# Optimization experiments

Measured on AMD Instinct MI355X. Metric: run time of the kernel, lower is better.

The kernel has to match this reference:

```python
import jax, jax.numpy as jnp
import numpy as np

# RCGANConfig constants
D_X, D_EPS = 64, 16
A_VOCAB, A_EMB = 100, 32
T_VOCAB, T_EMB = 4, 16
D_H = 128
D_IN = A_EMB + T_EMB + D_X + D_EPS + 1  # 129 (use_prev_y adds 1)


def setup_inputs() -> dict:
    key = jax.random.key(0)
    ks = jax.random.split(key, 20)
    B, T = 1024, 256
    s = 0.05
    x = jax.random.normal(ks[0], (B, D_X), jnp.float32)
    a = jax.random.randint(ks[1], (B, T), 0, A_VOCAB, jnp.int32)
    t = jax.random.randint(ks[2], (B, T), 0, T_VOCAB, jnp.int32)
    y = (jax.random.uniform(ks[3], (B, T)) < 0.5).astype(jnp.float32)
    mask = jnp.ones((B, T), jnp.float32)
    eps = jax.random.normal(ks[4], (B, T, D_EPS), jnp.float32)
    # parameters
    Wx = jax.random.normal(ks[5], (D_X, D_X), jnp.float32) * s
    bx = jnp.zeros((D_X,), jnp.float32)
    Ea = jax.random.normal(ks[6], (A_VOCAB, A_EMB), jnp.float32) * s
    Et = jax.random.normal(ks[7], (T_VOCAB, T_EMB), jnp.float32) * s
    Wih = jax.random.normal(ks[8], (3 * D_H, D_IN), jnp.float32) * s
    Whh = jax.random.normal(ks[9], (3 * D_H, D_H), jnp.float32) * s
    bih = jnp.zeros((3 * D_H,), jnp.float32)
    bhh = jnp.zeros((3 * D_H,), jnp.float32)
    W0 = jax.random.normal(ks[10], (D_H, D_X + D_EPS), jnp.float32) * s
    b0 = jnp.zeros((D_H,), jnp.float32)
    Wy = jax.random.normal(ks[11], (1, D_H), jnp.float32) * s
    by = jnp.zeros((1,), jnp.float32)
    return {"x": x, "a": a, "t": t, "y": y, "mask": mask, "eps": eps,
            "Wx": Wx, "bx": bx, "Ea": Ea, "Et": Et, "Wih": Wih, "Whh": Whh,
            "bih": bih, "bhh": bhh, "W0": W0, "b0": b0, "Wy": Wy, "by": by}


def reference(x, a, t, y, mask, eps, Wx, bx, Ea, Et, Wih, Whh, bih, bhh, W0, b0, Wy, by):
    # teacher_forcing path, rnn='gru', use_prev_y=True, y provided, stochastic_y=False
    B, T = a.shape
    x_enc = x @ Wx.T + bx                                        # [B, d_x] (constant per step)
    h0 = jnp.tanh(jnp.concatenate([x_enc, eps[:, 0, :]], -1) @ W0.T + b0)  # [B, d_h]
    # prev_y: zeros at t=0, then detached teacher signal y[:, t-1]
    prev_y = jnp.concatenate(
        [jnp.zeros((B, 1), y.dtype), jax.lax.stop_gradient(y[:, :-1])], axis=1)[..., None]  # [B,T,1]
    a_enc = Ea[a]                                                # [B,T,a_emb]
    t_enc = Et[t]                                                # [B,T,t_emb]
    inp = jnp.concatenate(
        [a_enc, t_enc, jnp.broadcast_to(x_enc[:, None, :], (B, T, x_enc.shape[-1])), eps, prev_y],
        axis=-1)                                                 # [B,T,d_in]
    gates_x = inp @ Wih.T + bih                                  # [B,T,3*d_h] precomputed input gates

    def step(h, gx):
        gh = h @ Whh.T + bhh
        gx_r, gx_z, gx_n = jnp.split(gx, 3, axis=-1)
        gh_r, gh_z, gh_n = jnp.split(gh, 3, axis=-1)
        r = jax.nn.sigmoid(gx_r + gh_r)
        z = jax.nn.sigmoid(gx_z + gh_z)
        n = jnp.tanh(gx_n + r * gh_n)
        h_new = (1.0 - z) * n + z * h
        return h_new, h_new

    _, hs = jax.lax.scan(step, h0, jnp.swapaxes(gates_x, 0, 1))  # hs: [T,B,d_h]
    hs = jnp.swapaxes(hs, 0, 1)                                  # [B,T,d_h]
    logits = hs @ Wy.T + by                                      # [B,T,1]
    prob = jax.nn.sigmoid(logits)
    m = mask[..., None]
    logits_o = m * logits + (1.0 - m) * jax.lax.stop_gradient(logits)
    y_o = m * prob + (1.0 - m) * jax.lax.stop_gradient(prob)
    # stacked: [..., 0] = y_logits, [..., 1] = y
    return jnp.concatenate([logits_o, y_o], axis=-1)             # [B,T,2]
```

## Files before the change

kernel.cpp:

```cpp
#include <hip/hip_runtime.h>
#include <hip/hip_bf16.h>

typedef __attribute__((ext_vector_type(8))) short bfrag;
typedef __attribute__((ext_vector_type(4))) float ffrag;

#define NB 1024
#define NT 256

#define KSIG -1.44269504f
#define KTAN -2.88539008f

static __device__ __forceinline__ float fast_rcp(float x) { return __builtin_amdgcn_rcpf(x); }
static __device__ __forceinline__ float sigm(float x) {
  return fast_rcp(1.f + __builtin_amdgcn_exp2f(-1.44269504f * x));
}
static __device__ __forceinline__ float sigm_pre(float s) {
  return fast_rcp(1.f + __builtin_amdgcn_exp2f(s));
}
static __device__ __forceinline__ float tanh_pre(float s) {
  return __builtin_fmaf(2.f, fast_rcp(1.f + __builtin_amdgcn_exp2f(s)), -1.f);
}
static __device__ __forceinline__ float tanh_f(float x) {
  return __builtin_fmaf(2.f, fast_rcp(1.f + __builtin_amdgcn_exp2f(-2.88539008f * x)), -1.f);
}
static __device__ __forceinline__ float bf2f(__hip_bfloat16 v) { return __bfloat162float(v); }
static __device__ __forceinline__ short f2bs(float f) {
  __hip_bfloat16 h = __float2bfloat16(f);
  return *reinterpret_cast<short*>(&h);
}
static __device__ __forceinline__ void barrier_lgkm() {
  asm volatile("s_waitcnt lgkmcnt(0)\n\ts_barrier" ::: "memory");
}

__global__ __launch_bounds__(512, 2) void gru_kernel(
    const float* __restrict__ x,
    const int* __restrict__ a_ids,
    const int* __restrict__ t_ids,
    const float* __restrict__ y,
    const float* __restrict__ eps,
    const float* __restrict__ Wx,
    const float* __restrict__ bx,
    const float* __restrict__ Ea,
    const float* __restrict__ Et,
    const float* __restrict__ Wih,
    const float* __restrict__ Whh,
    const float* __restrict__ bih,
    const float* __restrict__ bhh,
    const float* __restrict__ W0,
    const float* __restrict__ b0g,
    const float* __restrict__ Wy,
    const float* __restrict__ by,
    float* __restrict__ out)
{
  __shared__ __align__(16) __hip_bfloat16 h_bf[2][16][136];
  __shared__ __align__(16) __hip_bfloat16 Ea_s[100][40];
  __shared__ __align__(16) __hip_bfloat16 Et_s[4][16];
  __shared__ float prevy_s[2][16];
  __shared__ float bsum_r[128], bsum_z[128], bihn_s[128], bhhn_s[128];
  __shared__ float wprev_s[384];
  __shared__ __align__(16) char uni[38912];
  unsigned short* id_s    = (unsigned short*)(uni);
  __hip_bfloat16* eps_ch  = (__hip_bfloat16*)(uni + 8192);
  float*          y_ch    = (float*)(uni + 32768);
  __hip_bfloat16* Wxb     = (__hip_bfloat16*)(uni);
  __hip_bfloat16* W0b     = (__hip_bfloat16*)(uni + 8192);
  float*          x_s     = (float*)(uni + 28672);
  float*          eps0s   = (float*)(uni + 32832);
  float*          xe_s    = (float*)(uni + 33920);
  float*          h0f     = (float*)(uni);

  const int tid = threadIdx.x;
  const int w = tid >> 6, l = tid & 63;
  const int lmod = l & 15, ldiv = l >> 4;
  const int i_own = 16 * w + lmod;
  const int b0 = blockIdx.x * 16;

  if (tid < 128) {
    bsum_r[tid] = KSIG * (bih[tid] + bhh[tid]);
    bsum_z[tid] = KSIG * (bih[128 + tid] + bhh[128 + tid]);
    bihn_s[tid] = KTAN * bih[256 + tid];
    bhhn_s[tid] = KTAN * bhh[256 + tid];
  }
  if (tid < 384) wprev_s[tid] = ((tid < 256) ? KSIG : KTAN) * Wih[tid * 129 + 128];
  for (int j = tid; j < 3200; j += 512) {
    int r = j >> 5, c = j & 31;
    Ea_s[r][c] = __float2bfloat16(Ea[j]);
  }
  if (tid < 64) ((__hip_bfloat16*)Et_s)[tid] = __float2bfloat16(Et[tid]);
  for (int j = tid; j < 4096; j += 512)  Wxb[j] = __float2bfloat16(Wx[j]);
  for (int j = tid; j < 10240; j += 512) W0b[j] = __float2bfloat16(W0[j]);
  for (int j = tid; j < 1024; j += 512) {
    int r = j >> 6, c = j & 63;
    x_s[r * 65 + c] = x[(b0 + r) * 64 + c];
  }
  if (tid < 256) {
    int r = tid >> 4, c = tid & 15;
    eps0s[r * 17 + c] = eps[((b0 + r) * NT) * 16 + c];
  }
  const float by_f = by[0];

  bfrag Bh[3][4], Bi[3][2];
  #pragma unroll
  for (int g = 0; g < 3; g++) {
    const float sg = (g < 2) ? KSIG : KTAN;
    int n = (g * 8 + w) * 16 + lmod;
    #pragma unroll
    for (int kc = 0; kc < 4; kc++) {
      int k = kc * 32 + ldiv * 8;
      const float* wh = Whh + n * 128 + k;
      float4 h0v = *reinterpret_cast<const float4*>(wh);
      float4 h1v = *reinterpret_cast<const float4*>(wh + 4);
      bfrag th = {f2bs(sg * h0v.x), f2bs(sg * h0v.y), f2bs(sg * h0v.z), f2bs(sg * h0v.w),
                  f2bs(sg * h1v.x), f2bs(sg * h1v.y), f2bs(sg * h1v.z), f2bs(sg * h1v.w)};
      Bh[g][kc] = th;
    }
    #pragma unroll
    for (int kc = 0; kc < 2; kc++) {
      bfrag ti;
      #pragma unroll
      for (int j = 0; j < 8; j++) {
        int dk = kc * 32 + ldiv * 8 + j;
        int col = dk < 48 ? dk : dk + 64;
        ti[j] = f2bs(sg * Wih[n * 129 + col]);
      }
      Bi[g][kc] = ti;
    }
  }
  bfrag Bl[4];
  if (w == 7) {
    #pragma unroll
    for (int kc = 0; kc < 4; kc++) {
      bfrag bt;
      #pragma unroll
      for (int j = 0; j < 8; j++)
        bt[j] = (lmod == 0) ? f2bs(Wy[kc * 32 + ldiv * 8 + j]) : (short)0;
      Bl[kc] = bt;
    }
  }
  __syncthreads();

  for (int j = tid; j < 1024; j += 512) {
    int r = j & 15, i = j >> 4;
    float acc = bx[i];
    #pragma unroll 8
    for (int k = 0; k < 64; k++) acc += x_s[r * 65 + k] * bf2f(Wxb[i * 64 + k]);
    xe_s[r * 65 + i] = acc;
    h_bf[1][r][i] = __float2bfloat16(acc);
  }
  __syncthreads();

  for (int j = tid; j < 2048; j += 512) {
    int r = j & 15, o = j >> 4;
    float acc = b0g[o];
    #pragma unroll 8
    for (int k = 0; k < 64; k++) acc += xe_s[r * 65 + k] * bf2f(W0b[o * 80 + k]);
    #pragma unroll
    for (int k = 0; k < 16; k++) acc += eps0s[r * 17 + k] * bf2f(W0b[o * 80 + 64 + k]);
    h0f[r * 128 + o] = tanh_f(acc);
  }

  ffrag gxc[3];
  {
    ffrag z = {0.f, 0.f, 0.f, 0.f};
    gxc[0] = z; gxc[1] = z; gxc[2] = z;
    #pragma unroll
    for (int kc = 0; kc < 2; kc++) {
      bfrag axd = *reinterpret_cast<const bfrag*>(&h_bf[1][lmod][kc * 32 + ldiv * 8]);
      #pragma unroll
      for (int g = 0; g < 3; g++) {
        const float sg = (g < 2) ? KSIG : KTAN;
        int n = (g * 8 + w) * 16 + lmod;
        const float* wi = Wih + n * 129 + 48 + kc * 32 + ldiv * 8;
        bfrag bt;
        #pragma unroll
        for (int j = 0; j < 8; j++) bt[j] = f2bs(sg * wi[j]);
        gxc[g] = __builtin_amdgcn_mfma_f32_16x16x32_bf16(axd, bt, gxc[g], 0, 0, 0);
      }
    }
    float brf = bsum_r[i_own], bzf = bsum_z[i_own], bn1 = bihn_s[i_own];
    #pragma unroll
    for (int q = 0; q < 4; q++) {
      gxc[0][q] += brf;
      gxc[1][q] += bzf;
      gxc[2][q] += bn1;
    }
  }
  __syncthreads();

  float h_reg[4];
  #pragma unroll
  for (int q = 0; q < 4; q++) {
    int row = ldiv * 4 + q;
    float hv = h0f[row * 128 + i_own];
    h_reg[q] = hv;
    h_bf[0][row][i_own] = __float2bfloat16(hv);
  }
  __syncthreads();

  for (int j = tid; j < 4096; j += 512) {
    int r = j >> 8, t = j & 255;
    unsigned short v = (unsigned short)(a_ids[(b0 + r) * NT + t] |
                                        (t_ids[(b0 + r) * NT + t] << 8));
    id_s[t * 16 + r] = v;
  }
  {
    int r = tid >> 5, sub = tid & 31;
    const float* p = eps + ((b0 + r) * NT) * 16 + sub * 8;
    float4 eA = *reinterpret_cast<const float4*>(p);
    float4 eB = *reinterpret_cast<const float4*>(p + 4);
    int toff = sub >> 1, c8 = (sub & 1) * 8;
    bfrag e = {f2bs(eA.x), f2bs(eA.y), f2bs(eA.z), f2bs(eA.w),
               f2bs(eB.x), f2bs(eB.y), f2bs(eB.z), f2bs(eB.w)};
    *reinterpret_cast<bfrag*>(&eps_ch[(toff * 16 + r) * 24 + c8]) = e;
    if (tid < 64) {
      int r2 = tid >> 2, s2 = tid & 3;
      float4 yv = *reinterpret_cast<const float4*>(y + (b0 + r2) * NT + s2 * 4);
      *reinterpret_cast<float4*>(&y_ch[r2 * 16 + s2 * 4]) = yv;
    }
  }
  if (tid < 16) prevy_s[0][tid] = 0.f;
  const float wpr = wprev_s[i_own], wpz = wprev_s[128 + i_own], wpn = wprev_s[256 + i_own];
  const float bn2 = bhhn_s[i_own];
  const char* const ea_base  = (const char*)Ea_s + ldiv * 16;
  const char* const et_base  = (const char*)Et_s + ldiv * 16;
  const char* const eps_base = (const char*)eps_ch + lmod * 48 + (ldiv - 2) * 16;
  __syncthreads();

  ffrag pa0 = gxc[0], pa1 = gxc[1], pa2 = gxc[2];
  {
    int id = id_s[lmod];
    int aid = id & 127, tv = id >> 8;
    bfrag axA = *reinterpret_cast<const bfrag*>(ea_base + aid * 80);
    const char* etp = et_base + tv * 32;
    const char* epp = eps_base;
    bfrag axB = *reinterpret_cast<const bfrag*>(ldiv < 2 ? etp : epp);
    pa0 = __builtin_amdgcn_mfma_f32_16x16x32_bf16(axA, Bi[0][0], pa0, 0, 0, 0);
    pa1 = __builtin_amdgcn_mfma_f32_16x16x32_bf16(axA, Bi[1][0], pa1, 0, 0, 0);
    pa2 = __builtin_amdgcn_mfma_f32_16x16x32_bf16(axA, Bi[2][0], pa2, 0, 0, 0);
    pa0 = __builtin_amdgcn_mfma_f32_16x16x32_bf16(axB, Bi[0][1], pa0, 0, 0, 0);
    pa1 = __builtin_amdgcn_mfma_f32_16x16x32_bf16(axB, Bi[1][1], pa1, 0, 0, 0);
    pa2 = __builtin_amdgcn_mfma_f32_16x16x32_bf16(axB, Bi[2][1], pa2, 0, 0, 0);
  }

  for (int t = 0; t < NT; t++) {
    const int buf = t & 1, nbuf = buf ^ 1;

    const bool ck = ((t & 15) == 0) && (t + 16 < NT);
    float4 eA, eB, yv;
    const int cr = tid >> 5, csub = tid & 31;
    if (ck) {
      const float* p = eps + ((b0 + cr) * NT + t + 16) * 16 + csub * 8;
      eA = *reinterpret_cast<const float4*>(p);
      eB = *reinterpret_cast<const float4*>(p + 4);
      if (tid < 64) {
        int r2 = tid >> 2, s2 = tid & 3;
        yv = *reinterpret_cast<const float4*>(y + (b0 + r2) * NT + t + 16 + s2 * 4);
      }
    }

    ffrag anh, agl;
    #pragma unroll
    for (int q = 0; q < 4; q++) anh[q] = bn2;
    if (w == 7) {
      #pragma unroll
      for (int q = 0; q < 4; q++) agl[q] = by_f;
    }
    #pragma unroll
    for (int kc = 0; kc < 4; kc++) {
      bfrag ah = *reinterpret_cast<const bfrag*>(&h_bf[buf][lmod][kc * 32 + ldiv * 8]);
      pa0 = __builtin_amdgcn_mfma_f32_16x16x32_bf16(ah, Bh[0][kc], pa0, 0, 0, 0);
      pa1 = __builtin_amdgcn_mfma_f32_16x16x32_bf16(ah, Bh[1][kc], pa1, 0, 0, 0);
      anh = __builtin_amdgcn_mfma_f32_16x16x32_bf16(ah, Bh[2][kc], anh, 0, 0, 0);
      if (w == 7)
        agl = __builtin_amdgcn_mfma_f32_16x16x32_bf16(ah, Bl[kc], agl, 0, 0, 0);
    }

    if (tid >= 384 && tid < 400) {
      int r = tid - 384;
      prevy_s[nbuf][r] = y_ch[((t >> 4) & 1) * 256 + r * 16 + (t & 15)];
    }

    if (w == 7 && t > 0 && lmod == 0) {
      #pragma unroll
      for (int q = 0; q < 4; q++) {
        int row = ldiv * 4 + q;
        float lg = agl[q];
        float2 v;
        v.x = lg;
        v.y = sigm(lg);
        *reinterpret_cast<float2*>(out + ((b0 + row) * NT + (t - 1)) * 2) = v;
      }
    }

    #pragma unroll
    for (int q = 0; q < 4; q++) {
      int row = ldiv * 4 + q;
      float py = prevy_s[buf][row];
      float rv = sigm_pre(__builtin_fmaf(py, wpr, pa0[q]));
      float zv = sigm_pre(__builtin_fmaf(py, wpz, pa1[q]));
      float nv = tanh_pre(__builtin_fmaf(rv, anh[q], __builtin_fmaf(py, wpn, pa2[q])));
      float hn = __builtin_fmaf(zv, h_reg[q] - nv, nv);
      h_reg[q] = hn;
      h_bf[nbuf][row][i_own] = __float2bfloat16(hn);
    }

    if (t + 1 < NT) {
      const int tn = t + 1;
      const int ebase = (((tn >> 4) & 1) * 16 + (tn & 15)) * 16;
      int id = id_s[tn * 16 + lmod];
      int aid = id & 127, tv = id >> 8;
      bfrag axA = *reinterpret_cast<const bfrag*>(ea_base + aid * 80);
      const char* etp = et_base + tv * 32;
      const char* epp = eps_base + ebase * 48;
      bfrag axB = *reinterpret_cast<const bfrag*>(ldiv < 2 ? etp : epp);
      pa0 = gxc[0]; pa1 = gxc[1]; pa2 = gxc[2];
      pa0 = __builtin_amdgcn_mfma_f32_16x16x32_bf16(axA, Bi[0][0], pa0, 0, 0, 0);
      pa1 = __builtin_amdgcn_mfma_f32_16x16x32_bf16(axA, Bi[1][0], pa1, 0, 0, 0);
      pa2 = __builtin_amdgcn_mfma_f32_16x16x32_bf16(axA, Bi[2][0], pa2, 0, 0, 0);
      pa0 = __builtin_amdgcn_mfma_f32_16x16x32_bf16(axB, Bi[0][1], pa0, 0, 0, 0);
      pa1 = __builtin_amdgcn_mfma_f32_16x16x32_bf16(axB, Bi[1][1], pa1, 0, 0, 0);
      pa2 = __builtin_amdgcn_mfma_f32_16x16x32_bf16(axB, Bi[2][1], pa2, 0, 0, 0);
    }

    if (ck) {
      int cb2 = ((t >> 4) + 1) & 1;
      int toff = csub >> 1, c8 = (csub & 1) * 8;
      bfrag e = {f2bs(eA.x), f2bs(eA.y), f2bs(eA.z), f2bs(eA.w),
                 f2bs(eB.x), f2bs(eB.y), f2bs(eB.z), f2bs(eB.w)};
      *reinterpret_cast<bfrag*>(&eps_ch[((cb2 * 16 + toff) * 16 + cr) * 24 + c8]) = e;
      if (tid < 64) {
        int r2 = tid >> 2, s2 = tid & 3;
        *reinterpret_cast<float4*>(&y_ch[cb2 * 256 + r2 * 16 + s2 * 4]) = yv;
      }
    }

    barrier_lgkm();
  }

  if (w == 7) {
    ffrag agl;
    #pragma unroll
    for (int q = 0; q < 4; q++) agl[q] = by_f;
    #pragma unroll
    for (int kc = 0; kc < 4; kc++) {
      bfrag ah = *reinterpret_cast<const bfrag*>(&h_bf[0][lmod][kc * 32 + ldiv * 8]);
      agl = __builtin_amdgcn_mfma_f32_16x16x32_bf16(ah, Bl[kc], agl, 0, 0, 0);
    }
    if (lmod == 0) {
      #pragma unroll
      for (int q = 0; q < 4; q++) {
        int row = ldiv * 4 + q;
        float lg = agl[q];
        float2 v;
        v.x = lg;
        v.y = sigm(lg);
        *reinterpret_cast<float2*>(out + ((b0 + row) * NT + 255) * 2) = v;
      }
    }
  }
}

extern "C" void kernel_launch(void* const* d_in, const int* in_sizes, int n_in,
                              void* d_out, int out_size, void* d_ws, size_t ws_size,
                              hipStream_t stream) {
  const float* x   = (const float*)d_in[0];
  const int*   a   = (const int*)d_in[1];
  const int*   tt  = (const int*)d_in[2];
  const float* y   = (const float*)d_in[3];
  const float* eps = (const float*)d_in[5];
  const float* Wx  = (const float*)d_in[6];
  const float* bx  = (const float*)d_in[7];
  const float* Ea  = (const float*)d_in[8];
  const float* Et  = (const float*)d_in[9];
  const float* Wih = (const float*)d_in[10];
  const float* Whh = (const float*)d_in[11];
  const float* bih = (const float*)d_in[12];
  const float* bhh = (const float*)d_in[13];
  const float* W0  = (const float*)d_in[14];
  const float* b0  = (const float*)d_in[15];
  const float* Wy  = (const float*)d_in[16];
  const float* by  = (const float*)d_in[17];
  float* out = (float*)d_out;

  gru_kernel<<<NB / 16, 512, 0, stream>>>(x, a, tt, y, eps, Wx, bx, Ea, Et,
                                          Wih, Whh, bih, bhh, W0, b0, Wy, by, out);
}
```

Before: 347.3 us.

## Process 8 batch rows per block to double block count across CUs

Each block now handles 8 batch rows instead of 16, so the launch has twice as many blocks (128 instead of 64) and more of the GPU's CUs get work. The 16-row MFMA tiles stay the same, so the upper 8 rows are padded with zeros and half of every MFMA is wasted. All staging buffers, index math and the gate-update loop are shrunk or guarded to the 8-row layout. The sequential per-step latency is unchanged, but the parallelism across CUs roughly doubles, which fits a latency-bound recurrence.

```diff
diff --git a/kernel.cpp b/kernel.cpp
--- a/kernel.cpp
+++ b/kernel.cpp
@@ -6,6 +6,7 @@
 
 #define NB 1024
 #define NT 256
+#define RB 8
 
 #define KSIG -1.44269504f
 #define KTAN -2.88539008f
@@ -55,26 +56,27 @@
   __shared__ __align__(16) __hip_bfloat16 h_bf[2][16][136];
   __shared__ __align__(16) __hip_bfloat16 Ea_s[100][40];
   __shared__ __align__(16) __hip_bfloat16 Et_s[4][16];
-  __shared__ float prevy_s[2][16];
+  __shared__ float prevy_s[2][RB];
   __shared__ float bsum_r[128], bsum_z[128], bihn_s[128], bhhn_s[128];
   __shared__ float wprev_s[384];
-  __shared__ __align__(16) char uni[38912];
+  __shared__ __align__(16) char uni[33408];
   unsigned short* id_s    = (unsigned short*)(uni);
-  __hip_bfloat16* eps_ch  = (__hip_bfloat16*)(uni + 8192);
-  float*          y_ch    = (float*)(uni + 32768);
+  __hip_bfloat16* eps_ch  = (__hip_bfloat16*)(uni + 4096);
+  float*          y_ch    = (float*)(uni + 16384);
   __hip_bfloat16* Wxb     = (__hip_bfloat16*)(uni);
   __hip_bfloat16* W0b     = (__hip_bfloat16*)(uni + 8192);
   float*          x_s     = (float*)(uni + 28672);
-  float*          eps0s   = (float*)(uni + 32832);
-  float*          xe_s    = (float*)(uni + 33920);
+  float*          eps0s   = (float*)(uni + 30752);
+  float*          xe_s    = (float*)(uni + 31296);
   float*          h0f     = (float*)(uni);
 
   const int tid = threadIdx.x;
   const int w = tid >> 6, l = tid & 63;
   const int lmod = l & 15, ldiv = l >> 4;
   const int i_own = 16 * w + lmod;
-  const int b0 = blockIdx.x * 16;
-
+  const int b0 = blockIdx.x * RB;
+
+  for (int j = tid; j < 1088; j += 512) ((unsigned long long*)h_bf)[j] = 0ULL;
   if (tid < 128) {
     bsum_r[tid] = KSIG * (bih[tid] + bhh[tid]);
     bsum_z[tid] = KSIG * (bih[128 + tid] + bhh[128 + tid]);
@@ -89,11 +91,11 @@
   if (tid < 64) ((__hip_bfloat16*)Et_s)[tid] = __float2bfloat16(Et[tid]);
   for (int j = tid; j < 4096; j += 512)  Wxb[j] = __float2bfloat16(Wx[j]);
   for (int j = tid; j < 10240; j += 512) W0b[j] = __float2bfloat16(W0[j]);
-  for (int j = tid; j < 1024; j += 512) {
-    int r = j >> 6, c = j & 63;
+  if (tid < 512) {
+    int r = tid >> 6, c = tid & 63;
     x_s[r * 65 + c] = x[(b0 + r) * 64 + c];
   }
-  if (tid < 256) {
+  if (tid < 128) {
     int r = tid >> 4, c = tid & 15;
     eps0s[r * 17 + c] = eps[((b0 + r) * NT) * 16 + c];
   }
@@ -139,8 +141,8 @@
   }
   __syncthreads();
 
-  for (int j = tid; j < 1024; j += 512) {
-    int r = j & 15, i = j >> 4;
+  if (tid < 512) {
+    int r = tid & 7, i = tid >> 3;
     float acc = bx[i];
     #pragma unroll 8
     for (int k = 0; k < 64; k++) acc += x_s[r * 65 + k] * bf2f(Wxb[i * 64 + k]);
@@ -149,8 +151,8 @@
   }
   __syncthreads();
 
-  for (int j = tid; j < 2048; j += 512) {
-    int r = j & 15, o = j >> 4;
+  for (int j = tid; j < 1024; j += 512) {
+    int r = j & 7, o = j >> 3;
     float acc = b0g[o];
     #pragma unroll 8
     for (int k = 0; k < 64; k++) acc += xe_s[r * 65 + k] * bf2f(W0b[o * 80 + k]);
@@ -187,23 +189,25 @@
   }
   __syncthreads();
 
-  float h_reg[4];
-  #pragma unroll
-  for (int q = 0; q < 4; q++) {
-    int row = ldiv * 4 + q;
-    float hv = h0f[row * 128 + i_own];
-    h_reg[q] = hv;
-    h_bf[0][row][i_own] = __float2bfloat16(hv);
-  }
-  __syncthreads();
-
-  for (int j = tid; j < 4096; j += 512) {
+  float h_reg[4] = {0.f, 0.f, 0.f, 0.f};
+  if (ldiv < 2) {
+    #pragma unroll
+    for (int q = 0; q < 4; q++) {
+      int row = ldiv * 4 + q;
+      float hv = h0f[row * 128 + i_own];
+      h_reg[q] = hv;
+      h_bf[0][row][i_own] = __float2bfloat16(hv);
+    }
+  }
+  __syncthreads();
+
+  for (int j = tid; j < 2048; j += 512) {
     int r = j >> 8, t = j & 255;
     unsigned short v = (unsigned short)(a_ids[(b0 + r) * NT + t] |
                                         (t_ids[(b0 + r) * NT + t] << 8));
-    id_s[t * 16 + r] = v;
-  }
-  {
+    id_s[t * RB + r] = v;
+  }
+  if (tid < 256) {
     int r = tid >> 5, sub = tid & 31;
     const float* p = eps + ((b0 + r) * NT) * 16 + sub * 8;
     float4 eA = *reinterpret_cast<const float4*>(p);
@@ -211,24 +215,24 @@
     int toff = sub >> 1, c8 = (sub & 1) * 8;
     bfrag e = {f2bs(eA.x), f2bs(eA.y), f2bs(eA.z), f2bs(eA.w),
                f2bs(eB.x), f2bs(eB.y), f2bs(eB.z), f2bs(eB.w)};
-    *reinterpret_cast<bfrag*>(&eps_ch[(toff * 16 + r) * 24 + c8]) = e;
-    if (tid < 64) {
+    *reinterpret_cast<bfrag*>(&eps_ch[((0 * 16 + toff) * RB + r) * 24 + c8]) = e;
+    if (tid < 32) {
       int r2 = tid >> 2, s2 = tid & 3;
       float4 yv = *reinterpret_cast<const float4*>(y + (b0 + r2) * NT + s2 * 4);
       *reinterpret_cast<float4*>(&y_ch[r2 * 16 + s2 * 4]) = yv;
     }
   }
-  if (tid < 16) prevy_s[0][tid] = 0.f;
+  if (tid < RB) prevy_s[0][tid] = 0.f;
   const float wpr = wprev_s[i_own], wpz = wprev_s[128 + i_own], wpn = wprev_s[256 + i_own];
   const float bn2 = bhhn_s[i_own];
   const char* const ea_base  = (const char*)Ea_s + ldiv * 16;
   const char* const et_base  = (const char*)Et_s + ldiv * 16;
-  const char* const eps_base = (const char*)eps_ch + lmod * 48 + (ldiv - 2) * 16;
+  const char* const eps_base = (const char*)eps_ch + (lmod & 7) * 48 + (ldiv - 2) * 16;
   __syncthreads();
 
   ffrag pa0 = gxc[0], pa1 = gxc[1], pa2 = gxc[2];
   {
-    int id = id_s[lmod];
+    int id = id_s[lmod & 7];
     int aid = id & 127, tv = id >> 8;
     bfrag axA = *reinterpret_cast<const bfrag*>(ea_base + aid * 80);
     const char* etp = et_base + tv * 32;
@@ -248,11 +252,11 @@
     const bool ck = ((t & 15) == 0) && (t + 16 < NT);
     float4 eA, eB, yv;
     const int cr = tid >> 5, csub = tid & 31;
-    if (ck) {
+    if (ck && tid < 256) {
       const float* p = eps + ((b0 + cr) * NT + t + 16) * 16 + csub * 8;
       eA = *reinterpret_cast<const float4*>(p);
       eB = *reinterpret_cast<const float4*>(p + 4);
-      if (tid < 64) {
+      if (tid < 32) {
         int r2 = tid >> 2, s2 = tid & 3;
         yv = *reinterpret_cast<const float4*>(y + (b0 + r2) * NT + t + 16 + s2 * 4);
       }
@@ -275,12 +279,12 @@
         agl = __builtin_amdgcn_mfma_f32_16x16x32_bf16(ah, Bl[kc], agl, 0, 0, 0);
     }
 
-    if (tid >= 384 && tid < 400) {
+    if (tid >= 384 && tid < 384 + RB) {
       int r = tid - 384;
-      prevy_s[nbuf][r] = y_ch[((t >> 4) & 1) * 256 + r * 16 + (t & 15)];
-    }
-
-    if (w == 7 && t > 0 && lmod == 0) {
+      prevy_s[nbuf][r] = y_ch[((t >> 4) & 1) * (RB * 16) + r * 16 + (t & 15)];
+    }
+
+    if (w == 7 && t > 0 && lmod == 0 && ldiv < 2) {
       #pragma unroll
       for (int q = 0; q < 4; q++) {
         int row = ldiv * 4 + q;
@@ -292,22 +296,24 @@
       }
     }
 
-    #pragma unroll
-    for (int q = 0; q < 4; q++) {
-      int row = ldiv * 4 + q;
-      float py = prevy_s[buf][row];
-      float rv = sigm_pre(__builtin_fmaf(py, wpr, pa0[q]));
-      float zv = sigm_pre(__builtin_fmaf(py, wpz, pa1[q]));
-      float nv = tanh_pre(__builtin_fmaf(rv, anh[q], __builtin_fmaf(py, wpn, pa2[q])));
-      float hn = __builtin_fmaf(zv, h_reg[q] - nv, nv);
-      h_reg[q] = hn;
-      h_bf[nbuf][row][i_own] = __float2bfloat16(hn);
+    if (ldiv < 2) {
+      #pragma unroll
+      for (int q = 0; q < 4; q++) {
+        int row = ldiv * 4 + q;
+        float py = prevy_s[buf][row];
+        float rv = sigm_pre(__builtin_fmaf(py, wpr, pa0[q]));
+        float zv = sigm_pre(__builtin_fmaf(py, wpz, pa1[q]));
+        float nv = tanh_pre(__builtin_fmaf(rv, anh[q], __builtin_fmaf(py, wpn, pa2[q])));
+        float hn = __builtin_fmaf(zv, h_reg[q] - nv, nv);
+        h_reg[q] = hn;
+        h_bf[nbuf][row][i_own] = __float2bfloat16(hn);
+      }
     }
 
     if (t + 1 < NT) {
       const int tn = t + 1;
-      const int ebase = (((tn >> 4) & 1) * 16 + (tn & 15)) * 16;
-      int id = id_s[tn * 16 + lmod];
+      const int ebase = (((tn >> 4) & 1) * 16 + (tn & 15)) * RB;
+      int id = id_s[tn * RB + (lmod & 7)];
       int aid = id & 127, tv = id >> 8;
       bfrag axA = *reinterpret_cast<const bfrag*>(ea_base + aid * 80);
       const char* etp = et_base + tv * 32;
@@ -322,15 +328,15 @@
       pa2 = __builtin_amdgcn_mfma_f32_16x16x32_bf16(axB, Bi[2][1], pa2, 0, 0, 0);
     }
 
-    if (ck) {
+    if (ck && tid < 256) {
       int cb2 = ((t >> 4) + 1) & 1;
       int toff = csub >> 1, c8 = (csub & 1) * 8;
       bfrag e = {f2bs(eA.x), f2bs(eA.y), f2bs(eA.z), f2bs(eA.w),
                  f2bs(eB.x), f2bs(eB.y), f2bs(eB.z), f2bs(eB.w)};
-      *reinterpret_cast<bfrag*>(&eps_ch[((cb2 * 16 + toff) * 16 + cr) * 24 + c8]) = e;
-      if (tid < 64) {
+      *reinterpret_cast<bfrag*>(&eps_ch[((cb2 * 16 + toff) * RB + cr) * 24 + c8]) = e;
+      if (tid < 32) {
         int r2 = tid >> 2, s2 = tid & 3;
-        *reinterpret_cast<float4*>(&y_ch[cb2 * 256 + r2 * 16 + s2 * 4]) = yv;
+        *reinterpret_cast<float4*>(&y_ch[cb2 * (RB * 16) + r2 * 16 + s2 * 4]) = yv;
       }
     }
 
@@ -346,7 +352,7 @@
       bfrag ah = *reinterpret_cast<const bfrag*>(&h_bf[0][lmod][kc * 32 + ldiv * 8]);
       agl = __builtin_amdgcn_mfma_f32_16x16x32_bf16(ah, Bl[kc], agl, 0, 0, 0);
     }
-    if (lmod == 0) {
+    if (lmod == 0 && ldiv < 2) {
       #pragma unroll
       for (int q = 0; q < 4; q++) {
         int row = ldiv * 4 + q;
@@ -382,6 +388,6 @@
   const float* by  = (const float*)d_in[17];
   float* out = (float*)d_out;
 
-  gru_kernel<<<NB / 16, 512, 0, stream>>>(x, a, tt, y, eps, Wx, bx, Ea, Et,
+  gru_kernel<<<NB / RB, 512, 0, stream>>>(x, a, tt, y, eps, Wx, bx, Ea, Et,
                                           Wih, Whh, bih, bhh, W0, b0, Wy, by, out);
 }
```

Result: slower. 355.5 us (+2.4%).
